# Performance work log

Measured on AMD Instinct MI355X. Metric: run time of the kernel, lower is better.

## Reference

```python
import jax, jax.numpy as jnp
import numpy as np

NEG_SLOPE = 0.2
EPS = 1e-16

N_NODES = 100000
N_EDGES = 1600000
F_IN = 64
HID = 64
T_OUT = 1


def _gat_conv(x, src, dst, W, a_src, a_dst, b, n_nodes):
    # x: [N, Fin] -> h: [N, H]
    h = x @ W
    # per-node attention logits, then gather per-edge (PyG GATConv, heads=1)
    s_src = h @ a_src  # [N]
    s_dst = h @ a_dst  # [N]
    e = jax.nn.leaky_relu(s_src[src] + s_dst[dst], NEG_SLOPE)  # [E]
    # segment softmax over incoming edges of each destination node
    m = jax.ops.segment_max(e, dst, num_segments=n_nodes)  # [N]
    ex = jnp.exp(e - m[dst])
    denom = jax.ops.segment_sum(ex, dst, num_segments=n_nodes)  # [N]
    alpha = ex / (denom[dst] + EPS)  # [E]
    # weighted scatter-add aggregation
    out = jax.ops.segment_sum(alpha[:, None] * h[src], dst, num_segments=n_nodes)
    return out + b


def _add_self_loops(edge_index, n_nodes):
    loops = jnp.arange(n_nodes, dtype=edge_index.dtype)
    src = jnp.concatenate([edge_index[0], loops])
    dst = jnp.concatenate([edge_index[1], loops])
    return src, dst


def setup_inputs() -> dict:
    key = jax.random.key(0)
    ks = jax.random.split(key, 12)
    x = jax.random.normal(ks[0], (N_NODES, F_IN), dtype=jnp.float32)
    edge_index = jax.random.randint(ks[1], (2, N_EDGES), 0, N_NODES, dtype=jnp.int32)
    s1 = 1.0 / np.sqrt(F_IN)
    s2 = 1.0 / np.sqrt(HID)
    return {
        "x": x,
        "edge_index": edge_index,
        "W1": jax.random.normal(ks[2], (F_IN, HID), dtype=jnp.float32) * s1,
        "a_src1": jax.random.normal(ks[3], (HID,), dtype=jnp.float32) * s2,
        "a_dst1": jax.random.normal(ks[4], (HID,), dtype=jnp.float32) * s2,
        "b1": jnp.zeros((HID,), dtype=jnp.float32),
        "W2": jax.random.normal(ks[5], (HID, HID), dtype=jnp.float32) * s2,
        "a_src2": jax.random.normal(ks[6], (HID,), dtype=jnp.float32) * s2,
        "a_dst2": jax.random.normal(ks[7], (HID,), dtype=jnp.float32) * s2,
        "b2": jnp.zeros((HID,), dtype=jnp.float32),
        "Wl": jax.random.normal(ks[8], (HID, T_OUT), dtype=jnp.float32) * s2,
        "bl": jnp.zeros((T_OUT,), dtype=jnp.float32),
    }


def reference(x, edge_index, W1, a_src1, a_dst1, b1, W2, a_src2, a_dst2, b2, Wl, bl):
    n_nodes = x.shape[0]
    src, dst = _add_self_loops(edge_index, n_nodes)  # PyG add_self_loops=True
    h = _gat_conv(x, src, dst, W1, a_src1, a_dst1, b1, n_nodes)
    h = jnp.tanh(h)  # dropout is identity in eval mode
    h = _gat_conv(h, src, dst, W2, a_src2, a_dst2, b2, n_nodes)
    return h @ Wl + bl  # [N, 1]
```

## Files before the change

### kernel.cpp

```cpp
#include <hip/hip_runtime.h>

#define NN 100000
#define NE 1600000
#define ET (NE + NN)
#define NB 391
#define CAP 5120
#define BST 16
#define NBIN 256
#define NCHK (ET/8)
#define NTILE (NN/16)

typedef _Float16 f16;
typedef __attribute__((ext_vector_type(8))) _Float16 half8;
typedef __attribute__((ext_vector_type(4))) float f32x4;

__device__ __forceinline__ unsigned short hbits(float v){
    f16 h = (f16)v;
    return *(unsigned short*)&h;
}
__device__ __forceinline__ unsigned pk16(float a, float b){
    auto p = __builtin_amdgcn_cvt_pkrtz(a, b);
    return *(unsigned*)&p;
}
__device__ __forceinline__ float fast_tanh(float x){
    float e = __expf(2.f*x);
    return 1.f - __fdividef(2.f, e + 1.f);
}
__device__ __forceinline__ void fmix2(float& al, float& ah, unsigned h2, float a){
    asm("v_fma_mix_f32 %0, %2, %3, %0 op_sel_hi:[1,0,0]\n\t"
        "v_fma_mix_f32 %1, %2, %3, %1 op_sel:[1,0,0] op_sel_hi:[1,0,0]"
        : "+v"(al), "+v"(ah) : "v"(h2), "v"(a));
}

__global__ void __launch_bounds__(256) k_bin(const int* __restrict__ src,
        const int* __restrict__ dst, int* __restrict__ bcnt,
        int* __restrict__ binbuf){
    __shared__ int cnt[NB];
    __shared__ int cur[NB];
    int t = threadIdx.x;
    for(int i=t;i<NB;i+=256) cnt[i]=0;
    __syncthreads();
    for(int g = blockIdx.x*256 + t; g < NCHK; g += NBIN*256){
        if(g < NE/8){
            const uint4* dp = (const uint4*)(dst + g*8);
            uint4 d0 = dp[0], d1 = dp[1];
            atomicAdd(&cnt[d0.x>>8],1); atomicAdd(&cnt[d0.y>>8],1);
            atomicAdd(&cnt[d0.z>>8],1); atomicAdd(&cnt[d0.w>>8],1);
            atomicAdd(&cnt[d1.x>>8],1); atomicAdd(&cnt[d1.y>>8],1);
            atomicAdd(&cnt[d1.z>>8],1); atomicAdd(&cnt[d1.w>>8],1);
        } else {
            int n0 = g*8 - NE;
            #pragma unroll
            for(int i=0;i<8;i++) atomicAdd(&cnt[(n0+i)>>8],1);
        }
    }
    __syncthreads();
    for(int i=t;i<NB;i+=256){ int c=cnt[i]; cur[i] = c ? atomicAdd(&bcnt[i*BST], c) : 0; }
    __syncthreads();
    for(int g = blockIdx.x*256 + t; g < NCHK; g += NBIN*256){
        int s[8], d[8];
        if(g < NE/8){
            const uint4* sp = (const uint4*)(src + g*8);
            const uint4* dp = (const uint4*)(dst + g*8);
            uint4 s0 = sp[0], s1 = sp[1];
            uint4 d0 = dp[0], d1 = dp[1];
            s[0]=s0.x; s[1]=s0.y; s[2]=s0.z; s[3]=s0.w;
            s[4]=s1.x; s[5]=s1.y; s[6]=s1.z; s[7]=s1.w;
            d[0]=d0.x; d[1]=d0.y; d[2]=d0.z; d[3]=d0.w;
            d[4]=d1.x; d[5]=d1.y; d[6]=d1.z; d[7]=d1.w;
        } else {
            int n0 = g*8 - NE;
            #pragma unroll
            for(int i=0;i<8;i++){ s[i]=n0+i; d[i]=n0+i; }
        }
        #pragma unroll
        for(int i=0;i<8;i++){
            int b = d[i] >> 8;
            int pos = atomicAdd(&cur[b], 1);
            if(pos < CAP) binbuf[b*CAP + pos] = (s[i] << 8) | (d[i] & 255);
        }
    }
}

__global__ void __launch_bounds__(256) k_build(const int* __restrict__ bcnt,
        const int* __restrict__ binbuf, int* __restrict__ edge_src,
        int* __restrict__ rowst, int* __restrict__ deg){
    __shared__ int lsrc[CAP];
    __shared__ int ldeg[256], lscan[256], lcur[256], red[256];
    int b = blockIdx.x, t = threadIdx.x;
    int cnt = min(bcnt[b*BST], CAP);
    int part = 0;
    for(int i=t;i<b;i+=256) part += min(bcnt[i*BST], CAP);
    red[t] = part; __syncthreads();
    for(int off=128; off>=1; off>>=1){ if(t<off) red[t]+=red[t+off]; __syncthreads(); }
    int base = red[0];
    __syncthreads();
    ldeg[t] = 0; __syncthreads();
    const int* bb = binbuf + b*CAP;
    for(int i=t;i<cnt;i+=256) atomicAdd(&ldeg[bb[i] & 255], 1);
    __syncthreads();
    int dv = ldeg[t]; lscan[t] = dv; __syncthreads();
    for(int off=1; off<256; off<<=1){
        int u = (t>=off) ? lscan[t-off] : 0;
        __syncthreads(); lscan[t] += u; __syncthreads();
    }
    int excl = lscan[t] - dv; lcur[t] = excl;
    int node = b*256 + t;
    if(node < NN){ rowst[node] = base + excl; deg[node] = dv; }
    __syncthreads();
    for(int i=t;i<cnt;i+=256){
        int ent = bb[i];
        int pos = atomicAdd(&lcur[ent & 255], 1);
        lsrc[pos] = ent >> 8;
    }
    __syncthreads();
    for(int i=t;i<cnt;i+=256) edge_src[base+i] = lsrc[i];
}

template<int FPIN, int L2>
__global__ void __launch_bounds__(256) k_gemm(const void* __restrict__ xin,
        const float* __restrict__ W, const float* __restrict__ avs,
        const float* __restrict__ avd, const float* __restrict__ Wlv,
        f16* __restrict__ hb, float* __restrict__ ssrc,
        float* __restrict__ sdst, float* __restrict__ gsc){
    int tid = threadIdx.x, lane = tid & 63;
    int col = lane & 15, q = lane >> 4;
    half8 Bf[2][4];
    #pragma unroll
    for(int kh=0;kh<2;kh++){
        #pragma unroll
        for(int nb=0;nb<4;nb++){
            half8 b;
            #pragma unroll
            for(int j=0;j<8;j++){
                float w = W[(kh*32 + q*8 + j)*64 + nb*16 + col];
                b[j] = (f16)w;
            }
            Bf[kh][nb] = b;
        }
    }
    float as[4], ad[4], wl[4];
    #pragma unroll
    for(int nb=0;nb<4;nb++){
        as[nb] = avs[nb*16+col]; ad[nb] = avd[nb*16+col];
        wl[nb] = L2 ? Wlv[nb*16+col] : 0.f;
    }

    int gw = (blockIdx.x*256 + tid) >> 6;
    int nwaves = gridDim.x*4;
    for(int tile = gw; tile < NTILE; tile += nwaves){
        int n0 = tile*16;
        f32x4 acc[4];
        #pragma unroll
        for(int nb=0;nb<4;nb++) acc[nb] = (f32x4){0.f,0.f,0.f,0.f};
        #pragma unroll
        for(int kh=0;kh<2;kh++){
            half8 a;
            if(FPIN){
                const float4* xr = (const float4*)((const float*)xin
                                    + (size_t)(n0+col)*64 + kh*32 + q*8);
                float4 u = xr[0], v = xr[1];
                union { half8 h; uint4 u4; } A;
                A.u4.x = pk16(u.x, u.y);
                A.u4.y = pk16(u.z, u.w);
                A.u4.z = pk16(v.x, v.y);
                A.u4.w = pk16(v.z, v.w);
                a = A.h;
            } else {
                a = *(const half8*)((const f16*)xin
                                    + (size_t)(n0+col)*64 + kh*32 + q*8);
            }
            #pragma unroll
            for(int nb=0;nb<4;nb++)
                acc[nb] = __builtin_amdgcn_mfma_f32_16x16x32_f16(a, Bf[kh][nb], acc[nb], 0,0,0);
        }
        if(!L2){
            #pragma unroll
            for(int nb=0;nb<4;nb++){
                #pragma unroll
                for(int r=0;r<4;r++)
                    hb[(size_t)(n0 + q*4 + r)*64 + nb*16 + col] = (f16)acc[nb][r];
            }
        }
        #pragma unroll
        for(int r=0;r<4;r++){
            float ps = acc[0][r]*as[0] + acc[1][r]*as[1] + acc[2][r]*as[2] + acc[3][r]*as[3];
            float pd = acc[0][r]*ad[0] + acc[1][r]*ad[1] + acc[2][r]*ad[2] + acc[3][r]*ad[3];
            float pg = L2 ? (acc[0][r]*wl[0] + acc[1][r]*wl[1] + acc[2][r]*wl[2] + acc[3][r]*wl[3]) : 0.f;
            #pragma unroll
            for(int m=8;m>=1;m>>=1){
                ps += __shfl_xor(ps,m); pd += __shfl_xor(pd,m);
                if(L2) pg += __shfl_xor(pg,m);
            }
            if(col == 0){
                ssrc[n0 + q*4 + r] = ps; sdst[n0 + q*4 + r] = pd;
                if(L2) gsc[n0 + q*4 + r] = pg;
            }
        }
    }
}

__device__ __forceinline__ void node_full1(int node, int lane, int2* lp,
        const int* __restrict__ rowst, const int* __restrict__ deg,
        const int* __restrict__ edge_src, const float* __restrict__ ssrc,
        const float* __restrict__ sdst, const f16* __restrict__ hb,
        const float* __restrict__ bias, f16* __restrict__ out1b){
    int rs = rowst[node];
    int d  = deg[node];
    float sd = sdst[node];
    int g8 = lane >> 3;
    int c  = lane & 7;
    float a0=0.f,a1=0.f,a2=0.f,a3=0.f,a4=0.f,a5=0.f,a6=0.f,a7=0.f;

    float lmax = -1e30f;
    for(int j=lane; j<d; j+=64){
        int sj = edge_src[rs+j];
        float t = ssrc[sj] + sd;
        lmax = fmaxf(lmax, fmaxf(t, 0.2f*t));
    }
    #pragma unroll
    for(int m=32;m>=1;m>>=1) lmax = fmaxf(lmax, __shfl_xor(lmax,m));
    float lsum = 0.f;
    for(int j=lane; j<d; j+=64){
        int sj = edge_src[rs+j];
        float t = ssrc[sj] + sd;
        lsum += __expf(fmaxf(t, 0.2f*t) - lmax);
    }
    #pragma unroll
    for(int m=32;m>=1;m>>=1) lsum += __shfl_xor(lsum,m);
    float inv = 1.0f/(lsum + 1e-16f);
    for(int cb=0; cb<d; cb+=64){
        int s2 = 0; float al = 0.f;
        int j = cb + lane;
        if(j < d){
            s2 = edge_src[rs+j];
            float t = ssrc[s2] + sd;
            al = __expf(fmaxf(t, 0.2f*t) - lmax) * inv;
        }
        lp[lane] = make_int2(__float_as_int(al), s2);
        int dd = min(d - cb, 64);
        for(int i0=0; i0<dd; i0+=16){
            int2 e0 = lp[i0 + g8];
            int2 e1 = lp[i0 + 8 + g8];
            float f0 = __int_as_float(e0.x);
            float f1 = __int_as_float(e1.x);
            uint4 k0 = *(const uint4*)(hb + ((size_t)e0.y<<6) + (c<<3));
            uint4 k1 = *(const uint4*)(hb + ((size_t)e1.y<<6) + (c<<3));
            fmix2(a0,a1,k0.x,f0); fmix2(a2,a3,k0.y,f0);
            fmix2(a4,a5,k0.z,f0); fmix2(a6,a7,k0.w,f0);
            fmix2(a0,a1,k1.x,f1); fmix2(a2,a3,k1.y,f1);
            fmix2(a4,a5,k1.z,f1); fmix2(a6,a7,k1.w,f1);
        }
    }
    #pragma unroll
    for(int m=32;m>=8;m>>=1){
        a0 += __shfl_xor(a0,m); a1 += __shfl_xor(a1,m);
        a2 += __shfl_xor(a2,m); a3 += __shfl_xor(a3,m);
        a4 += __shfl_xor(a4,m); a5 += __shfl_xor(a5,m);
        a6 += __shfl_xor(a6,m); a7 += __shfl_xor(a7,m);
    }
    const float4* bp = (const float4*)bias;
    float4 bv0 = bp[c*2], bv1 = bp[c*2+1];
    if(g8 == 0){
        uint4 o;
        o.x = (unsigned)hbits(fast_tanh(a0+bv0.x)) | ((unsigned)hbits(fast_tanh(a1+bv0.y))<<16);
        o.y = (unsigned)hbits(fast_tanh(a2+bv0.z)) | ((unsigned)hbits(fast_tanh(a3+bv0.w))<<16);
        o.z = (unsigned)hbits(fast_tanh(a4+bv1.x)) | ((unsigned)hbits(fast_tanh(a5+bv1.y))<<16);
        o.w = (unsigned)hbits(fast_tanh(a6+bv1.z)) | ((unsigned)hbits(fast_tanh(a7+bv1.w))<<16);
        *(uint4*)(out1b + ((size_t)node<<6) + (c<<3)) = o;
    }
}

__global__ void __launch_bounds__(256) k_agg1(
        const int* __restrict__ rowst, const int* __restrict__ deg,
        const int* __restrict__ edge_src,
        const float* __restrict__ ssrc, const float* __restrict__ sdst,
        const f16* __restrict__ hb, const float* __restrict__ bias,
        f16* __restrict__ out1b){
    __shared__ int2 pairs[256];
    int tid = threadIdx.x;
    int wv   = (blockIdx.x*256 + tid) >> 6;
    int lane = tid & 63;
    if(wv*2 >= NN) return;
    int2* lp = pairs + (tid & 192);
    int half = lane >> 5, l = lane & 31;
    int node = wv*2 + half;

    int rs = rowst[node];
    int d  = deg[node];
    float sd = sdst[node];
    int dmax = max(d, __shfl_xor(d, 32));

    if(dmax <= 32){
        int s = 0; float pr = 0.f;
        if(l < d){
            s = edge_src[rs + l];
            float t = ssrc[s] + sd;
            t = fmaxf(t, 0.2f*t);
            pr = __expf(fminf(t, 80.f));
        }
        float sm = pr;
        #pragma unroll
        for(int m=16;m>=1;m>>=1) sm += __shfl_xor(sm,m);
        float alpha = pr * (1.0f/(sm + 1e-16f));
        lp[lane] = make_int2(__float_as_int(alpha), s);

        int g4 = l >> 3;
        int c  = l & 7;
        int base = half << 5;
        int nitw = (dmax + 7) >> 3;
        float F0[4], F1[4];
        uint4 K0[4], K1[4];
        #pragma unroll
        for(int it=0; it<4; it++){
            if(it < nitw){
                int2 e0 = lp[base + it*8 + g4];
                int2 e1 = lp[base + it*8 + 4 + g4];
                F0[it] = __int_as_float(e0.x);
                F1[it] = __int_as_float(e1.x);
                K0[it] = *(const uint4*)(hb + ((size_t)e0.y<<6) + (c<<3));
                K1[it] = *(const uint4*)(hb + ((size_t)e1.y<<6) + (c<<3));
            }
        }
        float a0=0.f,a1=0.f,a2=0.f,a3=0.f,a4=0.f,a5=0.f,a6=0.f,a7=0.f;
        #pragma unroll
        for(int it=0; it<4; it++){
            if(it < nitw){
                fmix2(a0,a1,K0[it].x,F0[it]); fmix2(a2,a3,K0[it].y,F0[it]);
                fmix2(a4,a5,K0[it].z,F0[it]); fmix2(a6,a7,K0[it].w,F0[it]);
                fmix2(a0,a1,K1[it].x,F1[it]); fmix2(a2,a3,K1[it].y,F1[it]);
                fmix2(a4,a5,K1[it].z,F1[it]); fmix2(a6,a7,K1[it].w,F1[it]);
            }
        }

        bool b3 = (l >> 3) & 1, b4 = (l >> 4) & 1;
        float u0 = b3 ? a4 : a0, v0 = b3 ? a0 : a4; u0 += __shfl_xor(v0, 8);
        float u1 = b3 ? a5 : a1, v1 = b3 ? a1 : a5; u1 += __shfl_xor(v1, 8);
        float u2 = b3 ? a6 : a2, v2 = b3 ? a2 : a6; u2 += __shfl_xor(v2, 8);
        float u3 = b3 ? a7 : a3, v3 = b3 ? a3 : a7; u3 += __shfl_xor(v3, 8);
        float w0 = b4 ? u2 : u0, z0 = b4 ? u0 : u2; w0 += __shfl_xor(z0, 16);
        float w1 = b4 ? u3 : u1, z1 = b4 ? u1 : u3; w1 += __shfl_xor(z1, 16);
        int ch0 = (c<<3) + ((int)b3<<2) + ((int)b4<<1);

        float2 bv = ((const float2*)bias)[ch0>>1];
        unsigned o = pk16(fast_tanh(w0 + bv.x), fast_tanh(w1 + bv.y));
        *(unsigned*)(out1b + ((size_t)node<<6) + ch0) = o;
    } else {
        node_full1(wv*2,   lane, lp, rowst, deg, edge_src, ssrc, sdst, hb, bias, out1b);
        node_full1(wv*2+1, lane, lp, rowst, deg, edge_src, ssrc, sdst, hb, bias, out1b);
    }
}

__global__ void __launch_bounds__(256) k_agg2(
        const int* __restrict__ rowst, const int* __restrict__ deg,
        const int* __restrict__ edge_src,
        const float* __restrict__ ssrc, const float* __restrict__ sdst,
        const float* __restrict__ gsc, const float* __restrict__ bias,
        const float* __restrict__ Wl, const float* __restrict__ bl,
        float* __restrict__ outF){
    int tid = threadIdx.x;
    int wv   = (blockIdx.x*256 + tid) >> 6;
    int lane = tid & 63;
    if(wv*2 >= NN) return;
    int half = lane >> 5, l = lane & 31;
    int node = wv*2 + half;

    float2 bv = ((const float2*)bias)[l];
    float2 wl = ((const float2*)Wl)[l];
    float rc = bv.x*wl.x + bv.y*wl.y;
    #pragma unroll
    for(int m=16;m>=1;m>>=1) rc += __shfl_xor(rc,m);

    int rs = rowst[node];
    int d  = deg[node];
    float sd = sdst[node];
    int dmax = max(d, __shfl_xor(d, 32));

    if(dmax <= 32){
        float pr = 0.f, gv = 0.f;
        if(l < d){
            int s = edge_src[rs + l];
            float t = ssrc[s] + sd;
            t = fmaxf(t, 0.2f*t);
            pr = __expf(fminf(t, 80.f));
            gv = gsc[s];
        }
        float sm = pr, num = pr*gv;
        #pragma unroll
        for(int m=16;m>=1;m>>=1){ sm += __shfl_xor(sm,m); num += __shfl_xor(num,m); }
        if(l == 0) outF[node] = num/(sm + 1e-16f) + rc + bl[0];
    } else {
        #pragma unroll 1
        for(int k=0;k<2;k++){
            int nd = wv*2 + k;
            int rs2 = rowst[nd], d2 = deg[nd];
            float sd2 = sdst[nd];
            float lmax = -1e30f;
            for(int j=lane; j<d2; j+=64){
                int sj = edge_src[rs2+j];
                float t = ssrc[sj] + sd2;
                lmax = fmaxf(lmax, fmaxf(t, 0.2f*t));
            }
            #pragma unroll
            for(int m=32;m>=1;m>>=1) lmax = fmaxf(lmax, __shfl_xor(lmax,m));
            float lsum = 0.f, lnum = 0.f;
            for(int j=lane; j<d2; j+=64){
                int sj = edge_src[rs2+j];
                float t = ssrc[sj] + sd2;
                float e = __expf(fmaxf(t, 0.2f*t) - lmax);
                lsum += e; lnum += e*gsc[sj];
            }
            #pragma unroll
            for(int m=32;m>=1;m>>=1){ lsum += __shfl_xor(lsum,m); lnum += __shfl_xor(lnum,m); }
            if(lane == 0) outF[nd] = lnum/(lsum + 1e-16f) + rc + bl[0];
        }
    }
}

extern "C" void kernel_launch(void* const* d_in, const int* in_sizes, int n_in,
                              void* d_out, int out_size, void* d_ws, size_t ws_size,
                              hipStream_t stream) {
    const float* x   = (const float*)d_in[0];
    const int*   ei  = (const int*)d_in[1];
    const float* W1  = (const float*)d_in[2];
    const float* as1 = (const float*)d_in[3];
    const float* ad1 = (const float*)d_in[4];
    const float* b1  = (const float*)d_in[5];
    const float* W2  = (const float*)d_in[6];
    const float* as2 = (const float*)d_in[7];
    const float* ad2 = (const float*)d_in[8];
    const float* b2  = (const float*)d_in[9];
    const float* Wl  = (const float*)d_in[10];
    const float* bl  = (const float*)d_in[11];
    float* out = (float*)d_out;

    const int* srcp = ei;
    const int* dstp = ei + NE;

    char* w = (char*)d_ws;
    int*   edge_src = (int*)w;  w += (size_t)ET*4;
    f16*   hb       = (f16*)w;  w += (size_t)NN*64*2;
    f16*   t1b      = (f16*)w;  w += (size_t)NN*64*2;
    int*   rowst    = (int*)w;  w += (size_t)NN*4;
    int*   deg      = (int*)w;  w += (size_t)NN*4;
    float* ssrc     = (float*)w; w += (size_t)NN*4;
    float* sdst     = (float*)w; w += (size_t)NN*4;
    float* gsc      = (float*)w; w += (size_t)NN*4;
    int*   bcnt     = (int*)w;  w += (size_t)NB*BST*4;
    int*   binbuf   = (int*)hb;

    const int nbG = 782;
    const int nbA = (NN/2 + 3)/4;

    (void)hipMemsetAsync(bcnt, 0, (size_t)NB*BST*4, stream);
    k_bin  <<<NBIN, 256, 0, stream>>>(srcp, dstp, bcnt, binbuf);
    k_build<<<NB,   256, 0, stream>>>(bcnt, binbuf, edge_src, rowst, deg);

    k_gemm<1,0><<<nbG, 256, 0, stream>>>((const void*)x, W1, as1, ad1,
                                         (const float*)nullptr, hb, ssrc, sdst,
                                         (float*)nullptr);
    k_agg1<<<nbA, 256, 0, stream>>>(rowst, deg, edge_src, ssrc, sdst, hb, b1, t1b);
    k_gemm<0,1><<<nbG, 256, 0, stream>>>((const void*)t1b, W2, as2, ad2, Wl,
                                         (f16*)nullptr, ssrc, sdst, gsc);
    k_agg2<<<nbA, 256, 0, stream>>>(rowst, deg, edge_src, ssrc, sdst, gsc,
                                    b2, Wl, bl, out);
}
```

Measured before the change: 197.4 us.

## Process four nodes per wavefront in layer-1 aggregation and pack row info

Row start and degree are merged into one int2 array, so each node's CSR info comes from a single load. The layer-1 aggregation kernel now handles four nodes per wavefront (two per half-wave, A and B) and issues all feature gathers for both before accumulating, which gives more memory-level parallelism. Edge indices and attention weights are now passed by lane shuffles rather than through LDS. The cost is higher register pressure from the eight uint4 buffers, which can lower occupancy, and half as many waves in the aggregation grid.

```diff
diff --git a/kernel.cpp b/kernel.cpp
--- a/kernel.cpp
+++ b/kernel.cpp
@@ -84,7 +84,7 @@
 
 __global__ void __launch_bounds__(256) k_build(const int* __restrict__ bcnt,
         const int* __restrict__ binbuf, int* __restrict__ edge_src,
-        int* __restrict__ rowst, int* __restrict__ deg){
+        int2* __restrict__ rd){
     __shared__ int lsrc[CAP];
     __shared__ int ldeg[256], lscan[256], lcur[256], red[256];
     int b = blockIdx.x, t = threadIdx.x;
@@ -106,7 +106,7 @@
     }
     int excl = lscan[t] - dv; lcur[t] = excl;
     int node = b*256 + t;
-    if(node < NN){ rowst[node] = base + excl; deg[node] = dv; }
+    if(node < NN) rd[node] = make_int2(base + excl, dv);
     __syncthreads();
     for(int i=t;i<cnt;i+=256){
         int ent = bb[i];
@@ -201,12 +201,12 @@
 }
 
 __device__ __forceinline__ void node_full1(int node, int lane, int2* lp,
-        const int* __restrict__ rowst, const int* __restrict__ deg,
-        const int* __restrict__ edge_src, const float* __restrict__ ssrc,
-        const float* __restrict__ sdst, const f16* __restrict__ hb,
-        const float* __restrict__ bias, f16* __restrict__ out1b){
-    int rs = rowst[node];
-    int d  = deg[node];
+        const int2* __restrict__ rd, const int* __restrict__ edge_src,
+        const float* __restrict__ ssrc, const float* __restrict__ sdst,
+        const f16* __restrict__ hb, const float* __restrict__ bias,
+        f16* __restrict__ out1b){
+    int2 r = rd[node];
+    int rs = r.x, d = r.y;
     float sd = sdst[node];
     int g8 = lane >> 3;
     int c  = lane & 7;
@@ -272,8 +272,7 @@
 }
 
 __global__ void __launch_bounds__(256) k_agg1(
-        const int* __restrict__ rowst, const int* __restrict__ deg,
-        const int* __restrict__ edge_src,
+        const int2* __restrict__ rd, const int* __restrict__ edge_src,
         const float* __restrict__ ssrc, const float* __restrict__ sdst,
         const f16* __restrict__ hb, const float* __restrict__ bias,
         f16* __restrict__ out1b){
@@ -281,79 +280,119 @@
     int tid = threadIdx.x;
     int wv   = (blockIdx.x*256 + tid) >> 6;
     int lane = tid & 63;
-    if(wv*2 >= NN) return;
+    if(wv*4 >= NN) return;
     int2* lp = pairs + (tid & 192);
     int half = lane >> 5, l = lane & 31;
-    int node = wv*2 + half;
-
-    int rs = rowst[node];
-    int d  = deg[node];
-    float sd = sdst[node];
-    int dmax = max(d, __shfl_xor(d, 32));
-
-    if(dmax <= 32){
-        int s = 0; float pr = 0.f;
-        if(l < d){
-            s = edge_src[rs + l];
-            float t = ssrc[s] + sd;
+    int nodeA = wv*4 + half;
+    int nodeB = wv*4 + 2 + half;
+
+    int2 rdA = rd[nodeA];
+    int2 rdB = rd[nodeB];
+    float sdA = sdst[nodeA], sdB = sdst[nodeB];
+    int dA2 = max(rdA.y, __shfl_xor(rdA.y, 32));
+    int dB2 = max(rdB.y, __shfl_xor(rdB.y, 32));
+
+    if(max(dA2, dB2) <= 32){
+        int sA = 0, sB = 0; float prA = 0.f, prB = 0.f;
+        if(l < rdA.y) sA = edge_src[rdA.x + l];
+        if(l < rdB.y) sB = edge_src[rdB.x + l];
+        if(l < rdA.y){
+            float t = ssrc[sA] + sdA;
             t = fmaxf(t, 0.2f*t);
-            pr = __expf(fminf(t, 80.f));
-        }
-        float sm = pr;
-        #pragma unroll
-        for(int m=16;m>=1;m>>=1) sm += __shfl_xor(sm,m);
-        float alpha = pr * (1.0f/(sm + 1e-16f));
-        lp[lane] = make_int2(__float_as_int(alpha), s);
-
-        int g4 = l >> 3;
-        int c  = l & 7;
-        int base = half << 5;
-        int nitw = (dmax + 7) >> 3;
-        float F0[4], F1[4];
-        uint4 K0[4], K1[4];
+            prA = __expf(fminf(t, 80.f));
+        }
+        if(l < rdB.y){
+            float t = ssrc[sB] + sdB;
+            t = fmaxf(t, 0.2f*t);
+            prB = __expf(fminf(t, 80.f));
+        }
+        float smA = prA, smB = prB;
+        #pragma unroll
+        for(int m=16;m>=1;m>>=1){ smA += __shfl_xor(smA,m); smB += __shfl_xor(smB,m); }
+        float alA = prA * (1.0f/(smA + 1e-16f));
+        float alB = prB * (1.0f/(smB + 1e-16f));
+
+        int g4 = l >> 3, c = l & 7;
+        int srcl = (half << 5) + g4;
+        int nitA = (dA2 + 7) >> 3, nitB = (dB2 + 7) >> 3;
+        uint4 K0a[4], K1a[4], K0b[4], K1b[4];
         #pragma unroll
         for(int it=0; it<4; it++){
-            if(it < nitw){
-                int2 e0 = lp[base + it*8 + g4];
-                int2 e1 = lp[base + it*8 + 4 + g4];
-                F0[it] = __int_as_float(e0.x);
-                F1[it] = __int_as_float(e1.x);
-                K0[it] = *(const uint4*)(hb + ((size_t)e0.y<<6) + (c<<3));
-                K1[it] = *(const uint4*)(hb + ((size_t)e1.y<<6) + (c<<3));
-            }
-        }
+            if(it < nitA){
+                int e0 = __shfl(sA, srcl + it*8);
+                int e1 = __shfl(sA, srcl + it*8 + 4);
+                K0a[it] = *(const uint4*)(hb + ((size_t)e0<<6) + (c<<3));
+                K1a[it] = *(const uint4*)(hb + ((size_t)e1<<6) + (c<<3));
+            }
+        }
+        #pragma unroll
+        for(int it=0; it<4; it++){
+            if(it < nitB){
+                int e0 = __shfl(sB, srcl + it*8);
+                int e1 = __shfl(sB, srcl + it*8 + 4);
+                K0b[it] = *(const uint4*)(hb + ((size_t)e0<<6) + (c<<3));
+                K1b[it] = *(const uint4*)(hb + ((size_t)e1<<6) + (c<<3));
+            }
+        }
+
         float a0=0.f,a1=0.f,a2=0.f,a3=0.f,a4=0.f,a5=0.f,a6=0.f,a7=0.f;
         #pragma unroll
         for(int it=0; it<4; it++){
-            if(it < nitw){
-                fmix2(a0,a1,K0[it].x,F0[it]); fmix2(a2,a3,K0[it].y,F0[it]);
-                fmix2(a4,a5,K0[it].z,F0[it]); fmix2(a6,a7,K0[it].w,F0[it]);
-                fmix2(a0,a1,K1[it].x,F1[it]); fmix2(a2,a3,K1[it].y,F1[it]);
-                fmix2(a4,a5,K1[it].z,F1[it]); fmix2(a6,a7,K1[it].w,F1[it]);
-            }
-        }
-
+            if(it < nitA){
+                float f0 = __shfl(alA, srcl + it*8);
+                float f1 = __shfl(alA, srcl + it*8 + 4);
+                fmix2(a0,a1,K0a[it].x,f0); fmix2(a2,a3,K0a[it].y,f0);
+                fmix2(a4,a5,K0a[it].z,f0); fmix2(a6,a7,K0a[it].w,f0);
+                fmix2(a0,a1,K1a[it].x,f1); fmix2(a2,a3,K1a[it].y,f1);
+                fmix2(a4,a5,K1a[it].z,f1); fmix2(a6,a7,K1a[it].w,f1);
+            }
+        }
         bool b3 = (l >> 3) & 1, b4 = (l >> 4) & 1;
-        float u0 = b3 ? a4 : a0, v0 = b3 ? a0 : a4; u0 += __shfl_xor(v0, 8);
-        float u1 = b3 ? a5 : a1, v1 = b3 ? a1 : a5; u1 += __shfl_xor(v1, 8);
-        float u2 = b3 ? a6 : a2, v2 = b3 ? a2 : a6; u2 += __shfl_xor(v2, 8);
-        float u3 = b3 ? a7 : a3, v3 = b3 ? a3 : a7; u3 += __shfl_xor(v3, 8);
-        float w0 = b4 ? u2 : u0, z0 = b4 ? u0 : u2; w0 += __shfl_xor(z0, 16);
-        float w1 = b4 ? u3 : u1, z1 = b4 ? u1 : u3; w1 += __shfl_xor(z1, 16);
         int ch0 = (c<<3) + ((int)b3<<2) + ((int)b4<<1);
-
         float2 bv = ((const float2*)bias)[ch0>>1];
-        unsigned o = pk16(fast_tanh(w0 + bv.x), fast_tanh(w1 + bv.y));
-        *(unsigned*)(out1b + ((size_t)node<<6) + ch0) = o;
+        {
+            float u0 = b3 ? a4 : a0, v0 = b3 ? a0 : a4; u0 += __shfl_xor(v0, 8);
+            float u1 = b3 ? a5 : a1, v1 = b3 ? a1 : a5; u1 += __shfl_xor(v1, 8);
+            float u2 = b3 ? a6 : a2, v2 = b3 ? a2 : a6; u2 += __shfl_xor(v2, 8);
+            float u3 = b3 ? a7 : a3, v3 = b3 ? a3 : a7; u3 += __shfl_xor(v3, 8);
+            float w0 = b4 ? u2 : u0, z0 = b4 ? u0 : u2; w0 += __shfl_xor(z0, 16);
+            float w1 = b4 ? u3 : u1, z1 = b4 ? u1 : u3; w1 += __shfl_xor(z1, 16);
+            unsigned o = pk16(fast_tanh(w0 + bv.x), fast_tanh(w1 + bv.y));
+            *(unsigned*)(out1b + ((size_t)nodeA<<6) + ch0) = o;
+        }
+
+        a0=0.f;a1=0.f;a2=0.f;a3=0.f;a4=0.f;a5=0.f;a6=0.f;a7=0.f;
+        #pragma unroll
+        for(int it=0; it<4; it++){
+            if(it < nitB){
+                float f0 = __shfl(alB, srcl + it*8);
+                float f1 = __shfl(alB, srcl + it*8 + 4);
+                fmix2(a0,a1,K0b[it].x,f0); fmix2(a2,a3,K0b[it].y,f0);
+                fmix2(a4,a5,K0b[it].z,f0); fmix2(a6,a7,K0b[it].w,f0);
+                fmix2(a0,a1,K1b[it].x,f1); fmix2(a2,a3,K1b[it].y,f1);
+                fmix2(a4,a5,K1b[it].z,f1); fmix2(a6,a7,K1b[it].w,f1);
+            }
+        }
+        {
+            float u0 = b3 ? a4 : a0, v0 = b3 ? a0 : a4; u0 += __shfl_xor(v0, 8);
+            float u1 = b3 ? a5 : a1, v1 = b3 ? a1 : a5; u1 += __shfl_xor(v1, 8);
+            float u2 = b3 ? a6 : a2, v2 = b3 ? a2 : a6; u2 += __shfl_xor(v2, 8);
+            float u3 = b3 ? a7 : a3, v3 = b3 ? a3 : a7; u3 += __shfl_xor(v3, 8);
+            float w0 = b4 ? u2 : u0, z0 = b4 ? u0 : u2; w0 += __shfl_xor(z0, 16);
+            float w1 = b4 ? u3 : u1, z1 = b4 ? u1 : u3; w1 += __shfl_xor(z1, 16);
+            unsigned o = pk16(fast_tanh(w0 + bv.x), fast_tanh(w1 + bv.y));
+            *(unsigned*)(out1b + ((size_t)nodeB<<6) + ch0) = o;
+        }
     } else {
-        node_full1(wv*2,   lane, lp, rowst, deg, edge_src, ssrc, sdst, hb, bias, out1b);
-        node_full1(wv*2+1, lane, lp, rowst, deg, edge_src, ssrc, sdst, hb, bias, out1b);
+        node_full1(wv*4,   lane, lp, rd, edge_src, ssrc, sdst, hb, bias, out1b);
+        node_full1(wv*4+1, lane, lp, rd, edge_src, ssrc, sdst, hb, bias, out1b);
+        node_full1(wv*4+2, lane, lp, rd, edge_src, ssrc, sdst, hb, bias, out1b);
+        node_full1(wv*4+3, lane, lp, rd, edge_src, ssrc, sdst, hb, bias, out1b);
     }
 }
 
 __global__ void __launch_bounds__(256) k_agg2(
-        const int* __restrict__ rowst, const int* __restrict__ deg,
-        const int* __restrict__ edge_src,
+        const int2* __restrict__ rd, const int* __restrict__ edge_src,
         const float* __restrict__ ssrc, const float* __restrict__ sdst,
         const float* __restrict__ gsc, const float* __restrict__ bias,
         const float* __restrict__ Wl, const float* __restrict__ bl,
@@ -371,8 +410,8 @@
     #pragma unroll
     for(int m=16;m>=1;m>>=1) rc += __shfl_xor(rc,m);
 
-    int rs = rowst[node];
-    int d  = deg[node];
+    int2 r = rd[node];
+    int rs = r.x, d = r.y;
     float sd = sdst[node];
     int dmax = max(d, __shfl_xor(d, 32));
 
@@ -393,7 +432,8 @@
         #pragma unroll 1
         for(int k=0;k<2;k++){
             int nd = wv*2 + k;
-            int rs2 = rowst[nd], d2 = deg[nd];
+            int2 r2 = rd[nd];
+            int rs2 = r2.x, d2 = r2.y;
             float sd2 = sdst[nd];
             float lmax = -1e30f;
             for(int j=lane; j<d2; j+=64){
@@ -441,27 +481,27 @@
     int*   edge_src = (int*)w;  w += (size_t)ET*4;
     f16*   hb       = (f16*)w;  w += (size_t)NN*64*2;
     f16*   t1b      = (f16*)w;  w += (size_t)NN*64*2;
-    int*   rowst    = (int*)w;  w += (size_t)NN*4;
-    int*   deg      = (int*)w;  w += (size_t)NN*4;
+    int2*  rd       = (int2*)w; w += (size_t)NN*8;
     float* ssrc     = (float*)w; w += (size_t)NN*4;
     float* sdst     = (float*)w; w += (size_t)NN*4;
     float* gsc      = (float*)w; w += (size_t)NN*4;
     int*   bcnt     = (int*)w;  w += (size_t)NB*BST*4;
     int*   binbuf   = (int*)hb;
 
-    const int nbG = 782;
-    const int nbA = (NN/2 + 3)/4;
+    const int nbG  = 782;
+    const int nbA1 = NN/16;
+    const int nbA2 = (NN/2 + 3)/4;
 
     (void)hipMemsetAsync(bcnt, 0, (size_t)NB*BST*4, stream);
     k_bin  <<<NBIN, 256, 0, stream>>>(srcp, dstp, bcnt, binbuf);
-    k_build<<<NB,   256, 0, stream>>>(bcnt, binbuf, edge_src, rowst, deg);
+    k_build<<<NB,   256, 0, stream>>>(bcnt, binbuf, edge_src, rd);
 
     k_gemm<1,0><<<nbG, 256, 0, stream>>>((const void*)x, W1, as1, ad1,
                                          (const float*)nullptr, hb, ssrc, sdst,
                                          (float*)nullptr);
-    k_agg1<<<nbA, 256, 0, stream>>>(rowst, deg, edge_src, ssrc, sdst, hb, b1, t1b);
+    k_agg1<<<nbA1, 256, 0, stream>>>(rd, edge_src, ssrc, sdst, hb, b1, t1b);
     k_gemm<0,1><<<nbG, 256, 0, stream>>>((const void*)t1b, W2, as2, ad2, Wl,
                                          (f16*)nullptr, ssrc, sdst, gsc);
-    k_agg2<<<nbA, 256, 0, stream>>>(rowst, deg, edge_src, ssrc, sdst, gsc,
-                                    b2, Wl, bl, out);
-}
+    k_agg2<<<nbA2, 256, 0, stream>>>(rd, edge_src, ssrc, sdst, gsc,
+                                     b2, Wl, bl, out);
+}
```

Result: slower. 210.2 us (+6.5%).
